# Kernel optimization log

Hardware: AMD Instinct MI355X
Metric: run time of the kernel (lower is better)

The kernel has to match this reference:

```python
import jax, jax.numpy as jnp
import numpy as np

E = 8        # num_experts (material buckets)
L1 = 3072    # input dim
L2 = 15
L3 = 32
RF = 32      # ROUTER_FEATURES_PER_PERSPECTIVE
B = 16384
AUX_ALPHA = 0.01
Z_ALPHA = 0.001
LOAD_FLOOR = 0.05
LOAD_CAP = 0.5
PROBE_ALPHA = 0.01
PROBE_TAU = 1.0
PROBE_THRESH = 0.05
TEACHER_ALPHA = 0.0   # initial value of _teacher_alpha buffer
SCORE_SCALE = 600.0
SQ_SCALE = 255.0 / 256.0


def setup_inputs() -> dict:
    key = jax.random.key(0)
    ks = jax.random.split(key, 12)
    x = jax.random.uniform(ks[0], (B, L1), dtype=jnp.float32)
    ls_indices = jax.random.randint(ks[1], (B,), 0, E)
    psqt = jax.random.normal(ks[2], (B,), dtype=jnp.float32)
    score_target = jax.random.normal(ks[3], (B,), dtype=jnp.float32)
    router_w = 0.1 * jax.random.normal(ks[4], (E, 2 * RF), dtype=jnp.float32)
    router_b = jnp.zeros((E,), dtype=jnp.float32)
    # effective (coalesced) expert params, per _expert_params view
    w1 = jax.random.normal(ks[5], (E, L2 + 1, L1), dtype=jnp.float32) / np.sqrt(L1)
    b1 = 0.01 * jax.random.normal(ks[6], (E, L2 + 1), dtype=jnp.float32)
    w2 = jax.random.normal(ks[7], (E, L3, 2 * L2), dtype=jnp.float32) / np.sqrt(2 * L2)
    b2 = 0.01 * jax.random.normal(ks[8], (E, L3), dtype=jnp.float32)
    w3 = jax.random.normal(ks[9], (E, 1, L3), dtype=jnp.float32) / np.sqrt(L3)
    b3 = jnp.zeros((E, 1), dtype=jnp.float32)  # output bias zeroed in __init__
    return {"x": x, "ls_indices": ls_indices, "psqt": psqt,
            "score_target": score_target, "router_w": router_w,
            "router_b": router_b, "w1": w1, "b1": b1, "w2": w2, "b2": b2,
            "w3": w3, "b3": b3}


def _forward(x, psqt, score_target, router_w, router_b, w1, b1, w2, b2, w3, b3, ls_indices):
    half = L1 // 2
    router_in = jnp.concatenate([x[:, :RF], x[:, half:half + RF]], axis=1)  # [B, 64]
    gate_logits = router_in @ router_w.T + router_b                          # [B, E]
    logp = jax.nn.log_softmax(gate_logits, axis=-1)
    gate_probs = jnp.exp(logp)
    expert_indices = jnp.argmax(gate_logits, axis=-1)                        # [B]

    teacher_ce = -jnp.mean(jnp.take_along_axis(logp, ls_indices[:, None], axis=1))
    frac = jnp.bincount(expert_indices, length=E).astype(gate_probs.dtype) / gate_probs.shape[0]
    avg_gate = gate_probs.mean(axis=0)
    load = avg_gate + jax.lax.stop_gradient(frac - avg_gate)
    floor_loss = jnp.mean(jnp.square(jnp.maximum(LOAD_FLOOR - load, 0.0)))
    cap_loss = jnp.mean(jnp.square(jnp.maximum(load - LOAD_CAP, 0.0)))
    aux_loss = floor_loss + cap_loss
    z_loss = jnp.mean(jnp.square(jax.nn.logsumexp(gate_logits, axis=-1)))

    # ---- all-experts stacked MLP (fusion target) ----
    l1c = jnp.einsum('bi,eoi->beo', x, w1) + b1          # [B, E, L2+1]
    a, a_skip = l1c[..., :L2], l1c[..., L2:]              # [B,E,L2], [B,E,1]
    h = jnp.clip(jnp.concatenate([a * a * SQ_SCALE, a], axis=-1), 0.0, 1.0)  # [B,E,2*L2]
    l2x = jnp.clip(jnp.einsum('bei,eoi->beo', h, w2) + b2, 0.0, 1.0)         # [B,E,L3]
    all_out = jnp.einsum('bei,eoi->beo', l2x, w3) + b3 + a_skip              # [B,E,1]

    # ---- probe loss ----
    probe_weight = PROBE_ALPHA * max(PROBE_THRESH - TEACHER_ALPHA, 0.0) / max(PROBE_THRESH, 1e-9)
    expert_out = (all_out[..., 0] + psqt[:, None]) * SCORE_SCALE             # [B, E]
    err = jnp.square(expert_out - score_target[:, None])
    err = err - err.min(axis=1, keepdims=True)
    pt = jax.nn.softmax(-jax.lax.stop_gradient(err) / PROBE_TAU, axis=-1)
    log_pt = jnp.log(jnp.maximum(pt, 1e-30))
    probe_loss = jnp.mean(jnp.sum(pt * (log_pt - logp), axis=-1))            # kl_div batchmean

    router_loss = (AUX_ALPHA * aux_loss + Z_ALPHA * z_loss
                   + TEACHER_ALPHA * teacher_ce + probe_weight * probe_loss)

    l3x = jnp.take_along_axis(all_out, expert_indices[:, None, None], axis=1)[:, 0, :]  # [B, 1]
    gp = jnp.take_along_axis(gate_probs, expert_indices[:, None], axis=1)               # [B, 1]
    l3x = l3x * (1.0 + gp - jax.lax.stop_gradient(gp))  # straight-through (training mode)
    return l3x, router_loss


def reference(x, ls_indices, psqt, score_target, router_w, router_b, w1, b1, w2, b2, w3, b3):
    return _forward(x, psqt, score_target, router_w, router_b, w1, b1, w2, b2, w3, b3, ls_indices)
```

## Files before the change

kernel.cpp:

```cpp
#include <hip/hip_runtime.h>
#include <math.h>

#define BATCH 16384
#define K_DIM 3072
#define KS    3
#define KSLICE 1024
#define BM    64
#define NITER 16

typedef float  f32x4  __attribute__((ext_vector_type(4)));
typedef __bf16 bf16x8 __attribute__((ext_vector_type(8)));
typedef unsigned int u32x4 __attribute__((ext_vector_type(4)));
typedef unsigned int u32x2 __attribute__((ext_vector_type(2)));

__device__ __forceinline__ unsigned short f2bf(float f) {
  union { float f; unsigned u; } v; v.f = f;
  unsigned u = v.u + 0x7fffu + ((v.u >> 16) & 1u);
  return (unsigned short)(u >> 16);
}

__global__ void cvt_kernel(const float* __restrict__ w1, unsigned short* __restrict__ o,
                           const float* __restrict__ w2, float* __restrict__ w2t) {
  if (blockIdx.x < 384) {
    int i = blockIdx.x * 256 + threadIdx.x;
    f32x4 v = ((const f32x4*)w1)[i];
    u32x2 p = { (unsigned)f2bf(v.x) | ((unsigned)f2bf(v.y) << 16),
                (unsigned)f2bf(v.z) | ((unsigned)f2bf(v.w) << 16) };
    ((u32x2*)o)[i] = p;
  } else {
    for (int j = threadIdx.x; j < 7680; j += 256) {
      int e = j / 960; int r = j - e * 960; int oo = r / 30; int ii = r - oo * 30;
      w2t[e * 960 + ii * 32 + oo] = w2[j];
    }
  }
}

__global__ __launch_bounds__(256, 3) void gemm_partial_kernel(
    const float* __restrict__ x, const unsigned short* __restrict__ w1bf,
    float* __restrict__ partial) {
  __shared__ __align__(16) unsigned short xs[64 * 72];
  __shared__ __align__(16) unsigned short wsd[128 * 72];

  const int tid = threadIdx.x;
  const int bm  = blockIdx.x / KS;
  const int ksl = blockIdx.x - bm * KS;
  const int m0  = bm * BM;
  const size_t k0 = (size_t)ksl * KSLICE;

  const int srow = tid >> 4;
  const int sc   = tid & 15;
  const float*          gx = x    + (size_t)(m0 + srow) * K_DIM + k0 + sc * 4;
  const unsigned short* gw = w1bf + (size_t)srow * K_DIM + k0 + sc * 4;
  const int sxo = srow * 72 + sc * 4;

  const int lane = tid & 63, wid = tid >> 6;
  const int m16 = lane & 15, q = lane >> 4;
  const int arow = (wid & 1) * 32;
  const int bcol = (wid >> 1) * 64;

  f32x4 acc[2][4];
#pragma unroll
  for (int i = 0; i < 2; ++i)
#pragma unroll
    for (int j = 0; j < 4; ++j) acc[i][j] = (f32x4){0.f, 0.f, 0.f, 0.f};

  f32x4 xv[4];
  u32x2 wv[8];
#pragma unroll
  for (int p = 0; p < 4; ++p) xv[p] = *(const f32x4*)(gx + (size_t)p * 16 * K_DIM);
#pragma unroll
  for (int p = 0; p < 8; ++p) wv[p] = *(const u32x2*)(gw + (size_t)p * 16 * K_DIM);

  for (int kt = 0; kt < NITER; ++kt) {
    __syncthreads();
#pragma unroll
    for (int p = 0; p < 4; ++p) {
      u32x2 pk = { (unsigned)f2bf(xv[p].x) | ((unsigned)f2bf(xv[p].y) << 16),
                   (unsigned)f2bf(xv[p].z) | ((unsigned)f2bf(xv[p].w) << 16) };
      *(u32x2*)&xs[sxo + p * 16 * 72] = pk;
    }
#pragma unroll
    for (int p = 0; p < 8; ++p)
      *(u32x2*)&wsd[sxo + p * 16 * 72] = wv[p];
    __syncthreads();
    if (kt < NITER - 1) {
      const size_t ko = (size_t)(kt + 1) * 64;
#pragma unroll
      for (int p = 0; p < 4; ++p) xv[p] = *(const f32x4*)(gx + (size_t)p * 16 * K_DIM + ko);
#pragma unroll
      for (int p = 0; p < 8; ++p) wv[p] = *(const u32x2*)(gw + (size_t)p * 16 * K_DIM + ko);
    }
#pragma unroll
    for (int ks2 = 0; ks2 < 2; ++ks2) {
      bf16x8 af[2];
#pragma unroll
      for (int i = 0; i < 2; ++i)
        af[i] = *(const bf16x8*)&xs[(arow + i * 16 + m16) * 72 + ks2 * 32 + q * 8];
#pragma unroll
      for (int j = 0; j < 4; ++j) {
        bf16x8 bf = *(const bf16x8*)&wsd[(bcol + j * 16 + m16) * 72 + ks2 * 32 + q * 8];
#pragma unroll
        for (int i = 0; i < 2; ++i)
          acc[i][j] = __builtin_amdgcn_mfma_f32_16x16x32_bf16(af[i], bf, acc[i][j], 0, 0, 0);
      }
    }
  }

  float* pb = partial + (size_t)ksl * (BATCH * 128);
#pragma unroll
  for (int i = 0; i < 2; ++i)
#pragma unroll
    for (int j = 0; j < 4; ++j)
#pragma unroll
      for (int r = 0; r < 4; ++r)
        pb[(size_t)(m0 + arow + i * 16 + q * 4 + r) * 128 + bcol + j * 16 + m16] = acc[i][j][r];
}

__global__ __launch_bounds__(256, 4) void moe_tail_kernel(
    const float* __restrict__ x, const float* __restrict__ partial,
    const float* __restrict__ b1, const float* __restrict__ w2t,
    const float* __restrict__ b2, const float* __restrict__ w3,
    const float* __restrict__ b3, const float* __restrict__ psqt,
    const float* __restrict__ st, const float* __restrict__ rw,
    const float* __restrict__ rb, float* __restrict__ out,
    float* __restrict__ accs) {
  __shared__ float rws_s[512];
  __shared__ int   hist_s[8];
  __shared__ float zsum_s, psum_s;

  const int tid = threadIdx.x;
  const int bm  = blockIdx.x;
  rws_s[tid] = rw[tid];
  rws_s[tid + 256] = rw[tid + 256];
  if (tid < 8) hist_s[tid] = 0;
  if (tid == 0) { zsum_s = 0.f; psum_s = 0.f; }
  __syncthreads();

  const int r = tid >> 3, e = tid & 7;
  const int bg = bm * 32 + r;
  const int lane = tid & 63, wid = tid >> 6;

  float a[16];
  {
    const size_t off = (size_t)bg * 128 + e * 16;
#pragma unroll
    for (int j4 = 0; j4 < 4; ++j4) {
      f32x4 s = *(const f32x4*)(partial + off + j4 * 4);
      s = s + *(const f32x4*)(partial + (size_t)BATCH * 128 + off + j4 * 4);
      s = s + *(const f32x4*)(partial + (size_t)2 * BATCH * 128 + off + j4 * 4);
      f32x4 bq = *(const f32x4*)(b1 + e * 16 + j4 * 4);
      s = s + bq;
      a[j4 * 4 + 0] = s.x; a[j4 * 4 + 1] = s.y; a[j4 * 4 + 2] = s.z; a[j4 * 4 + 3] = s.w;
    }
  }

  float logp_own; int cand;
  {
    const float* xrow = x + (size_t)bg * K_DIM;
    double l0 = (double)rb[e], l1 = 0.0;
#pragma unroll
    for (int c = 0; c < 32; c += 2) {
      l0 = fma((double)xrow[c],     (double)rws_s[e * 64 + c],     l0);
      l1 = fma((double)xrow[c + 1], (double)rws_s[e * 64 + c + 1], l1);
    }
#pragma unroll
    for (int c = 0; c < 32; c += 2) {
      l0 = fma((double)xrow[1536 + c],     (double)rws_s[e * 64 + 32 + c],     l0);
      l1 = fma((double)xrow[1536 + c + 1], (double)rws_s[e * 64 + 32 + c + 1], l1);
    }
    double l = l0 + l1;
    double mx = l;
    mx = fmax(mx, __shfl_xor(mx, 1));
    mx = fmax(mx, __shfl_xor(mx, 2));
    mx = fmax(mx, __shfl_xor(mx, 4));
    int cd = (l == mx) ? e : 8;
    cd = min(cd, __shfl_xor(cd, 1));
    cd = min(cd, __shfl_xor(cd, 2));
    cd = min(cd, __shfl_xor(cd, 4));
    cand = cd;
    double s = exp(l - mx);
    s += __shfl_xor(s, 1); s += __shfl_xor(s, 2); s += __shfl_xor(s, 4);
    double lse = mx + log(s);
    logp_own = (float)(l - lse);
    if (e == 0) atomicAdd(&zsum_s, (float)(lse * lse));
    if (e == cd) atomicAdd(&hist_s[cd], 1);
  }

  float h[30];
#pragma unroll
  for (int j = 0; j < 15; ++j) {
    float v = a[j];
    h[j]      = fminf(fmaxf(v * v * (255.0f / 256.0f), 0.f), 1.f);
    h[15 + j] = fminf(fmaxf(v, 0.f), 1.f);
  }

  float acc2[32];
  const f32x4* b2v = (const f32x4*)(b2 + e * 32);
#pragma unroll
  for (int o4 = 0; o4 < 8; ++o4) {
    f32x4 bq = b2v[o4];
    acc2[o4 * 4 + 0] = bq.x; acc2[o4 * 4 + 1] = bq.y;
    acc2[o4 * 4 + 2] = bq.z; acc2[o4 * 4 + 3] = bq.w;
  }
  const f32x4* wrow = (const f32x4*)(w2t + e * 960);
#pragma unroll
  for (int i = 0; i < 30; ++i) {
    float hv = h[i];
#pragma unroll
    for (int o4 = 0; o4 < 8; ++o4) {
      f32x4 wq = wrow[i * 8 + o4];
      acc2[o4 * 4 + 0] += hv * wq.x;
      acc2[o4 * 4 + 1] += hv * wq.y;
      acc2[o4 * 4 + 2] += hv * wq.z;
      acc2[o4 * 4 + 3] += hv * wq.w;
    }
  }

  float outv = b3[e] + a[15];
  const f32x4* w3v = (const f32x4*)(w3 + e * 32);
#pragma unroll
  for (int o4 = 0; o4 < 8; ++o4) {
    f32x4 wq = w3v[o4];
#pragma unroll
    for (int k = 0; k < 4; ++k) {
      float l2v = fminf(fmaxf(acc2[o4 * 4 + k], 0.f), 1.f);
      outv += l2v * ((const float*)&wq)[k];
    }
  }

  float eo  = (outv + psqt[bg]) * 600.0f;
  float dd  = eo - st[bg];
  float err = dd * dd;
  float mn = err;
  mn = fminf(mn, __shfl_xor(mn, 1));
  mn = fminf(mn, __shfl_xor(mn, 2));
  mn = fminf(mn, __shfl_xor(mn, 4));
  float wexp = expf(-(err - mn));
  float ssum = wexp;
  ssum += __shfl_xor(ssum, 1); ssum += __shfl_xor(ssum, 2); ssum += __shfl_xor(ssum, 4);
  float pt  = wexp / ssum;
  float lpt = logf(fmaxf(pt, 1e-30f));
  float term = pt * (lpt - logp_own);
  term += __shfl_xor(term, 1); term += __shfl_xor(term, 2); term += __shfl_xor(term, 4);
  float c1 = (e == 0) ? term : 0.f;
  c1 += __shfl_xor(c1, 8); c1 += __shfl_xor(c1, 16); c1 += __shfl_xor(c1, 32);
  if (lane == 0) atomicAdd(&psum_s, c1);

  if (e == cand) out[bg] = outv;

  __syncthreads();
  if (tid == 0) {
    atomicAdd(&accs[8], zsum_s);
    atomicAdd(&accs[9], psum_s);
  }
  if (tid < 8) atomicAdd(&accs[tid], (float)hist_s[tid]);
}

__global__ void finalize_kernel(const float* __restrict__ accs, float* __restrict__ out) {
  if (threadIdx.x == 0) {
    float fsum = 0.f;
    for (int e = 0; e < 8; ++e) {
      float frac = accs[e] * (1.0f / 16384.0f);
      float f = fmaxf(0.05f - frac, 0.f);
      float c = fmaxf(frac - 0.5f, 0.f);
      fsum += f * f + c * c;
    }
    float aux   = fsum * 0.125f;
    float z     = accs[8] * (1.0f / 16384.0f);
    float probe = accs[9] * (1.0f / 16384.0f);
    out[BATCH] = 0.01f * aux + 0.001f * z + 0.01f * probe;
  }
}

extern "C" void kernel_launch(void* const* d_in, const int* in_sizes, int n_in,
                              void* d_out, int out_size, void* d_ws, size_t ws_size,
                              hipStream_t stream) {
  const float* x    = (const float*)d_in[0];
  const float* psqt = (const float*)d_in[2];
  const float* st   = (const float*)d_in[3];
  const float* rw   = (const float*)d_in[4];
  const float* rb   = (const float*)d_in[5];
  const float* w1   = (const float*)d_in[6];
  const float* b1   = (const float*)d_in[7];
  const float* w2   = (const float*)d_in[8];
  const float* b2   = (const float*)d_in[9];
  const float* w3   = (const float*)d_in[10];
  const float* b3   = (const float*)d_in[11];
  float* out = (float*)d_out;

  unsigned short* w1bf = (unsigned short*)d_ws;
  float* w2t     = (float*)((char*)d_ws + 786432);
  float* accs    = (float*)((char*)d_ws + 786432 + 30720);
  float* partial = (float*)((char*)d_ws + 1048576);

  hipMemsetAsync(accs, 0, 16 * sizeof(float), stream);
  cvt_kernel<<<385, 256, 0, stream>>>(w1, w1bf, w2, w2t);
  gemm_partial_kernel<<<768, 256, 0, stream>>>(x, w1bf, partial);
  moe_tail_kernel<<<512, 256, 0, stream>>>(x, partial, b1, w2t, b2, w3, b3,
                                           psqt, st, rw, rb, out, accs);
  finalize_kernel<<<1, 1, 0, stream>>>(accs, out);
}
```

Baseline: 407.4 us.

## Rewrite GEMM as LDS-free register-direct MFMA with 4-way K split

The partial GEMM drops shared-memory staging. Each wave loads x rows and bf16 W1 rows straight into registers in MFMA fragment layout, double-buffers them, and computes 32 rows by all 128 columns across a 4-way K split. The tail kernel sums four partials and computes the softmax log-sum-exp in float instead of double. The accumulator memset is folded into the conversion kernel, removing one launch. Together these target barrier and LDS overhead, double-precision transcendental cost and launch overhead. The trade-offs are more partial-buffer traffic, uncoalesced strided global loads per lane and slightly lower precision in the router statistics.

```diff
diff --git a/kernel.cpp b/kernel.cpp
--- a/kernel.cpp
+++ b/kernel.cpp
@@ -3,14 +3,12 @@
 
 #define BATCH 16384
 #define K_DIM 3072
-#define KS    3
-#define KSLICE 1024
-#define BM    64
-#define NITER 16
+#define KS    4
+#define KSL   768
+#define NKT   24
 
 typedef float  f32x4  __attribute__((ext_vector_type(4)));
 typedef __bf16 bf16x8 __attribute__((ext_vector_type(8)));
-typedef unsigned int u32x4 __attribute__((ext_vector_type(4)));
 typedef unsigned int u32x2 __attribute__((ext_vector_type(2)));
 
 __device__ __forceinline__ unsigned short f2bf(float f) {
@@ -19,8 +17,18 @@
   return (unsigned short)(u >> 16);
 }
 
+__device__ __forceinline__ bf16x8 cvt8(f32x4 lo, f32x4 hi) {
+  union { unsigned u[4]; bf16x8 v; } r;
+  r.u[0] = (unsigned)f2bf(lo.x) | ((unsigned)f2bf(lo.y) << 16);
+  r.u[1] = (unsigned)f2bf(lo.z) | ((unsigned)f2bf(lo.w) << 16);
+  r.u[2] = (unsigned)f2bf(hi.x) | ((unsigned)f2bf(hi.y) << 16);
+  r.u[3] = (unsigned)f2bf(hi.z) | ((unsigned)f2bf(hi.w) << 16);
+  return r.v;
+}
+
 __global__ void cvt_kernel(const float* __restrict__ w1, unsigned short* __restrict__ o,
-                           const float* __restrict__ w2, float* __restrict__ w2t) {
+                           const float* __restrict__ w2, float* __restrict__ w2t,
+                           float* __restrict__ accs) {
   if (blockIdx.x < 384) {
     int i = blockIdx.x * 256 + threadIdx.x;
     f32x4 v = ((const f32x4*)w1)[i];
@@ -28,6 +36,7 @@
                 (unsigned)f2bf(v.z) | ((unsigned)f2bf(v.w) << 16) };
     ((u32x2*)o)[i] = p;
   } else {
+    if (threadIdx.x < 16) accs[threadIdx.x] = 0.f;
     for (int j = threadIdx.x; j < 7680; j += 256) {
       int e = j / 960; int r = j - e * 960; int oo = r / 30; int ii = r - oo * 30;
       w2t[e * 960 + ii * 32 + oo] = w2[j];
@@ -35,85 +44,72 @@
   }
 }
 
-__global__ __launch_bounds__(256, 3) void gemm_partial_kernel(
+__global__ __launch_bounds__(256, 2) void gemm_partial_kernel(
     const float* __restrict__ x, const unsigned short* __restrict__ w1bf,
     float* __restrict__ partial) {
-  __shared__ __align__(16) unsigned short xs[64 * 72];
-  __shared__ __align__(16) unsigned short wsd[128 * 72];
-
-  const int tid = threadIdx.x;
-  const int bm  = blockIdx.x / KS;
-  const int ksl = blockIdx.x - bm * KS;
-  const int m0  = bm * BM;
-  const size_t k0 = (size_t)ksl * KSLICE;
-
-  const int srow = tid >> 4;
-  const int sc   = tid & 15;
-  const float*          gx = x    + (size_t)(m0 + srow) * K_DIM + k0 + sc * 4;
-  const unsigned short* gw = w1bf + (size_t)srow * K_DIM + k0 + sc * 4;
-  const int sxo = srow * 72 + sc * 4;
-
-  const int lane = tid & 63, wid = tid >> 6;
-  const int m16 = lane & 15, q = lane >> 4;
-  const int arow = (wid & 1) * 32;
-  const int bcol = (wid >> 1) * 64;
-
-  f32x4 acc[2][4];
+  const int tid  = threadIdx.x;
+  const int bm   = blockIdx.x >> 2;
+  const int ks   = blockIdx.x & 3;
+  const int wrow = tid >> 6;
+  const int lane = tid & 63;
+  const int m16  = lane & 15, q = lane >> 4;
+  const int r0   = bm * 128 + wrow * 32;
+  const int k0   = ks * KSL;
+
+  const float* xp0 = x + (size_t)(r0 + m16) * K_DIM + k0 + q * 8;
+  const float* xp1 = xp0 + (size_t)16 * K_DIM;
+  const __bf16* wp = (const __bf16*)w1bf + (size_t)m16 * K_DIM + k0 + q * 8;
+
+  f32x4 acc[2][8];
 #pragma unroll
   for (int i = 0; i < 2; ++i)
 #pragma unroll
-    for (int j = 0; j < 4; ++j) acc[i][j] = (f32x4){0.f, 0.f, 0.f, 0.f};
-
-  f32x4 xv[4];
-  u32x2 wv[8];
-#pragma unroll
-  for (int p = 0; p < 4; ++p) xv[p] = *(const f32x4*)(gx + (size_t)p * 16 * K_DIM);
-#pragma unroll
-  for (int p = 0; p < 8; ++p) wv[p] = *(const u32x2*)(gw + (size_t)p * 16 * K_DIM);
-
-  for (int kt = 0; kt < NITER; ++kt) {
-    __syncthreads();
-#pragma unroll
-    for (int p = 0; p < 4; ++p) {
-      u32x2 pk = { (unsigned)f2bf(xv[p].x) | ((unsigned)f2bf(xv[p].y) << 16),
-                   (unsigned)f2bf(xv[p].z) | ((unsigned)f2bf(xv[p].w) << 16) };
-      *(u32x2*)&xs[sxo + p * 16 * 72] = pk;
-    }
-#pragma unroll
-    for (int p = 0; p < 8; ++p)
-      *(u32x2*)&wsd[sxo + p * 16 * 72] = wv[p];
-    __syncthreads();
-    if (kt < NITER - 1) {
-      const size_t ko = (size_t)(kt + 1) * 64;
-#pragma unroll
-      for (int p = 0; p < 4; ++p) xv[p] = *(const f32x4*)(gx + (size_t)p * 16 * K_DIM + ko);
-#pragma unroll
-      for (int p = 0; p < 8; ++p) wv[p] = *(const u32x2*)(gw + (size_t)p * 16 * K_DIM + ko);
-    }
-#pragma unroll
-    for (int ks2 = 0; ks2 < 2; ++ks2) {
-      bf16x8 af[2];
-#pragma unroll
-      for (int i = 0; i < 2; ++i)
-        af[i] = *(const bf16x8*)&xs[(arow + i * 16 + m16) * 72 + ks2 * 32 + q * 8];
-#pragma unroll
-      for (int j = 0; j < 4; ++j) {
-        bf16x8 bf = *(const bf16x8*)&wsd[(bcol + j * 16 + m16) * 72 + ks2 * 32 + q * 8];
-#pragma unroll
-        for (int i = 0; i < 2; ++i)
-          acc[i][j] = __builtin_amdgcn_mfma_f32_16x16x32_bf16(af[i], bf, acc[i][j], 0, 0, 0);
-      }
-    }
-  }
-
-  float* pb = partial + (size_t)ksl * (BATCH * 128);
+    for (int j = 0; j < 8; ++j) acc[i][j] = (f32x4){0.f, 0.f, 0.f, 0.f};
+
+  f32x4 a_cur[4];
+  bf16x8 b_cur[8];
+  a_cur[0] = *(const f32x4*)(xp0);
+  a_cur[1] = *(const f32x4*)(xp0 + 4);
+  a_cur[2] = *(const f32x4*)(xp1);
+  a_cur[3] = *(const f32x4*)(xp1 + 4);
+#pragma unroll
+  for (int j = 0; j < 8; ++j)
+    b_cur[j] = *(const bf16x8*)(wp + (size_t)j * 16 * K_DIM);
+
+  for (int kt = 0; kt < NKT; ++kt) {
+    f32x4 a_nxt[4];
+    bf16x8 b_nxt[8];
+    if (kt < NKT - 1) {
+      const int ko = (kt + 1) * 32;
+      a_nxt[0] = *(const f32x4*)(xp0 + ko);
+      a_nxt[1] = *(const f32x4*)(xp0 + ko + 4);
+      a_nxt[2] = *(const f32x4*)(xp1 + ko);
+      a_nxt[3] = *(const f32x4*)(xp1 + ko + 4);
+#pragma unroll
+      for (int j = 0; j < 8; ++j)
+        b_nxt[j] = *(const bf16x8*)(wp + (size_t)j * 16 * K_DIM + ko);
+    }
+    bf16x8 af0 = cvt8(a_cur[0], a_cur[1]);
+    bf16x8 af1 = cvt8(a_cur[2], a_cur[3]);
+#pragma unroll
+    for (int j = 0; j < 8; ++j) {
+      acc[0][j] = __builtin_amdgcn_mfma_f32_16x16x32_bf16(af0, b_cur[j], acc[0][j], 0, 0, 0);
+      acc[1][j] = __builtin_amdgcn_mfma_f32_16x16x32_bf16(af1, b_cur[j], acc[1][j], 0, 0, 0);
+    }
+#pragma unroll
+    for (int p = 0; p < 4; ++p) a_cur[p] = a_nxt[p];
+#pragma unroll
+    for (int j = 0; j < 8; ++j) b_cur[j] = b_nxt[j];
+  }
+
+  float* pb = partial + (size_t)ks * (BATCH * 128);
 #pragma unroll
   for (int i = 0; i < 2; ++i)
 #pragma unroll
-    for (int j = 0; j < 4; ++j)
+    for (int j = 0; j < 8; ++j)
 #pragma unroll
       for (int r = 0; r < 4; ++r)
-        pb[(size_t)(m0 + arow + i * 16 + q * 4 + r) * 128 + bcol + j * 16 + m16] = acc[i][j][r];
+        pb[(size_t)(r0 + i * 16 + q * 4 + r) * 128 + j * 16 + m16] = acc[i][j][r];
 }
 
 __global__ __launch_bounds__(256, 4) void moe_tail_kernel(
@@ -146,8 +142,9 @@
 #pragma unroll
     for (int j4 = 0; j4 < 4; ++j4) {
       f32x4 s = *(const f32x4*)(partial + off + j4 * 4);
-      s = s + *(const f32x4*)(partial + (size_t)BATCH * 128 + off + j4 * 4);
-      s = s + *(const f32x4*)(partial + (size_t)2 * BATCH * 128 + off + j4 * 4);
+#pragma unroll
+      for (int sl = 1; sl < KS; ++sl)
+        s = s + *(const f32x4*)(partial + (size_t)sl * BATCH * 128 + off + j4 * 4);
       f32x4 bq = *(const f32x4*)(b1 + e * 16 + j4 * 4);
       s = s + bq;
       a[j4 * 4 + 0] = s.x; a[j4 * 4 + 1] = s.y; a[j4 * 4 + 2] = s.z; a[j4 * 4 + 3] = s.w;
@@ -178,11 +175,15 @@
     cd = min(cd, __shfl_xor(cd, 2));
     cd = min(cd, __shfl_xor(cd, 4));
     cand = cd;
-    double s = exp(l - mx);
+    float d = (float)(l - mx);
+    float s = expf(d);
     s += __shfl_xor(s, 1); s += __shfl_xor(s, 2); s += __shfl_xor(s, 4);
-    double lse = mx + log(s);
-    logp_own = (float)(l - lse);
-    if (e == 0) atomicAdd(&zsum_s, (float)(lse * lse));
+    float lgs = logf(s);
+    logp_own = d - lgs;
+    if (e == 0) {
+      float lse = (float)mx + lgs;
+      atomicAdd(&zsum_s, lse * lse);
+    }
     if (e == cd) atomicAdd(&hist_s[cd], 1);
   }
 
@@ -293,9 +294,8 @@
   float* accs    = (float*)((char*)d_ws + 786432 + 30720);
   float* partial = (float*)((char*)d_ws + 1048576);
 
-  hipMemsetAsync(accs, 0, 16 * sizeof(float), stream);
-  cvt_kernel<<<385, 256, 0, stream>>>(w1, w1bf, w2, w2t);
-  gemm_partial_kernel<<<768, 256, 0, stream>>>(x, w1bf, partial);
+  cvt_kernel<<<385, 256, 0, stream>>>(w1, w1bf, w2, w2t, accs);
+  gemm_partial_kernel<<<512, 256, 0, stream>>>(x, w1bf, partial);
   moe_tail_kernel<<<512, 256, 0, stream>>>(x, partial, b1, w2t, b2, w3, b3,
                                            psqt, st, rw, rb, out, accs);
   finalize_kernel<<<1, 1, 0, stream>>>(accs, out);
```

After: 420.8 us. 1.03x slower.
